# Optimization experiments

Hardware: AMD Instinct MI355X
Metric: run time of the kernel (lower is better)

## Reference

```python
import jax, jax.numpy as jnp
import numpy as np

H_IMG, W_IMG = 160, 160
C1, C2, HEADS, NHOPS = 128, 256, 8, 2
N_NODES = H_IMG * W_IMG


def build_edges(H, W):
    # 3x3 neighborhood (excl. self) + skip edges (i+2,j),(i,j+2); self loops added once
    node = (np.arange(H)[:, None] * W + np.arange(W)[None, :])
    offsets = [(di, dj) for di in (-1, 0, 1) for dj in (-1, 0, 1) if (di, dj) != (0, 0)] + [(2, 0), (0, 2)]
    srcs, dsts = [], []
    for di, dj in offsets:
        i0, i1 = max(0, -di), H - max(0, di)
        j0, j1 = max(0, -dj), W - max(0, dj)
        srcs.append(node[i0:i1, j0:j1].ravel())
        dsts.append(node[i0 + di:i1 + di, j0 + dj:j1 + dj].ravel())
    n = np.arange(H * W)
    srcs.append(n); dsts.append(n)
    return (np.concatenate(srcs).astype(np.int32), np.concatenate(dsts).astype(np.int32))


def setup_inputs() -> dict:
    key = jax.random.key(0)
    ks = jax.random.split(key, 16)
    s = 0.05
    src_np, dst_np = build_edges(H_IMG, W_IMG)
    d = C2 // HEADS
    return {
        "x": jax.random.normal(ks[0], (1, C1, H_IMG, W_IMG), jnp.float32),
        "w_id": jax.random.normal(ks[1], (C2, C1), jnp.float32) * s,
        "w_in": jax.random.normal(ks[2], (C2, C1), jnp.float32) * s,
        "w_gat": jax.random.normal(ks[3], (NHOPS, C2, C2), jnp.float32) * s,
        "a_src": jax.random.normal(ks[4], (NHOPS, HEADS, d), jnp.float32) * s,
        "a_dst": jax.random.normal(ks[5], (NHOPS, HEADS, d), jnp.float32) * s,
        "gat_bias": jax.random.normal(ks[6], (NHOPS, C2), jnp.float32) * s,
        "bn_gamma": jax.random.uniform(ks[7], (NHOPS, C2), jnp.float32, 0.5, 1.5),
        "bn_beta": jax.random.normal(ks[8], (NHOPS, C2), jnp.float32) * s,
        "bn_mean": jax.random.normal(ks[9], (NHOPS, C2), jnp.float32) * s,
        "bn_var": jax.random.uniform(ks[10], (NHOPS, C2), jnp.float32, 0.5, 1.5),
        "w_out": jax.random.normal(ks[11], (C2, C2), jnp.float32) * s,
        "se_w1": jax.random.normal(ks[12], (C2 // 4, C2), jnp.float32) * s,
        "se_b1": jax.random.normal(ks[13], (C2 // 4,), jnp.float32) * s,
        "se_w2": jax.random.normal(ks[14], (C2, C2 // 4), jnp.float32) * s,
        "se_b2": jax.random.normal(ks[15], (C2,), jnp.float32) * s,
        "src": jnp.asarray(src_np),
        "dst": jnp.asarray(dst_np),
    }


def _gat(x, W, a_s, a_d, b, src, dst, N):
    heads, d = a_s.shape
    h = (x @ W.T).reshape(N, heads, d)                      # [N,H,D]
    al_s = jnp.einsum('nhd,hd->nh', h, a_s)                 # [N,H]
    al_d = jnp.einsum('nhd,hd->nh', h, a_d)
    e = jax.nn.leaky_relu(al_s[src] + al_d[dst], 0.2)       # [E,H]
    emax = jax.lax.stop_gradient(jax.ops.segment_max(e, dst, num_segments=N))
    ee = jnp.exp(e - emax[dst])
    denom = jax.ops.segment_sum(ee, dst, num_segments=N)
    alpha = ee / (denom[dst] + 1e-16)                       # segment softmax over incoming edges
    out = jax.ops.segment_sum(h[src] * alpha[..., None], dst, num_segments=N)
    return out.reshape(N, heads * d) + b


def _forward(x, w_id, w_in, w_gat, a_src, a_dst, gat_bias, bn_gamma, bn_beta,
             bn_mean, bn_var, w_out, se_w1, se_b1, se_w2, se_b2, src, dst):
    identity = jnp.einsum('bchw,oc->bohw', x, w_id)
    h = jnp.einsum('bchw,oc->bohw', x, w_in)
    B, C, H, W = h.shape
    N = B * H * W
    xf = h.transpose(0, 2, 3, 1).reshape(N, C)
    for l in range(NHOPS):
        res = xf
        g = _gat(xf, w_gat[l], a_src[l], a_dst[l], gat_bias[l], src, dst, N)
        g = (g - bn_mean[l]) * (bn_gamma[l] * jax.lax.rsqrt(bn_var[l] + 1e-5)) + bn_beta[l]
        xf = jax.nn.relu(g) + res
    y = xf.reshape(B, H, W, C).transpose(0, 3, 1, 2)
    y = jnp.einsum('bchw,oc->bohw', y, w_out)
    # SE block
    w = y.mean(axis=(2, 3))                                 # [B,C]
    w = jax.nn.relu(w @ se_w1.T + se_b1)
    w = jax.nn.sigmoid(w @ se_w2.T + se_b2)
    y = y * w[:, :, None, None]
    return y + identity


def reference(x, w_id, w_in, w_gat, a_src, a_dst, gat_bias, bn_gamma, bn_beta,
              bn_mean, bn_var, w_out, se_w1, se_b1, se_w2, se_b2, src, dst):
    return _forward(x, w_id, w_in, w_gat, a_src, a_dst, gat_bias, bn_gamma, bn_beta,
                    bn_mean, bn_var, w_out, se_w1, se_b1, se_w2, se_b2, src, dst)
```

## Files before the change

kernel.cpp:

```cpp
#include <hip/hip_runtime.h>

#define NN 25600
#define HH 160
#define WW 160
#define C2 256
#define MSLOTS 64

#define B_WIN   0
#define B_WID   32768
#define B_WGAT  65536
#define B_WOUT  196608
#define B_WEND  262144

#define C_BNA   0
#define C_BNB   512
#define C_ASRC  1024
#define C_ADST  1536
#define C_SEW1  2048
#define C_SEB1  18432
#define C_SEW2  18496
#define C_SEB2  34880
#define C_END   35136

typedef __attribute__((ext_vector_type(8))) short bfrag;
typedef __attribute__((ext_vector_type(4))) float ffrag;

__device__ __forceinline__ float b2f(unsigned short u) {
    union { unsigned int ui; float f; } v; v.ui = ((unsigned int)u) << 16; return v.f;
}
__device__ __forceinline__ unsigned short f2b(float f) {
    union { float f; unsigned int u; } v; v.f = f;
    unsigned int u = v.u;
    unsigned int r = (u + 0x7FFFu + ((u >> 16) & 1u)) >> 16;
    return (unsigned short)r;
}
__device__ __forceinline__ float lo16f(unsigned int w) {
    union { unsigned int ui; float f; } v; v.ui = w << 16; return v.f;
}
__device__ __forceinline__ float hi16f(unsigned int w) {
    union { unsigned int ui; float f; } v; v.ui = w & 0xFFFF0000u; return v.f;
}
__device__ __forceinline__ bool probe_f32(const unsigned short* __restrict__ x) {
    int l = threadIdx.x & 63;
    bool wild = false;
#pragma unroll
    for (int i = 0; i < 8; ++i) {
        float v = b2f(x[l * 8 + i]);
        wild |= !(fabsf(v) < 1e6f);
    }
    return __any(wild);
}
__device__ __forceinline__ float ldf(const void* p, long i, bool f32) {
    return f32 ? ((const float*)p)[i] : b2f(((const unsigned short*)p)[i]);
}

__device__ __forceinline__ void gemm_tile_ids(int bid, int& m0, int& o0) {
    int w = (bid & 7) * 200 + (bid >> 3);
    m0 = (w >> 2) * 64;
    o0 = (w & 3) * 64;
}

__device__ __forceinline__ const bfrag* fragp(const unsigned short* buf, int row, int c8) {
    return (const bfrag*)(buf + row * 64 + ((c8 ^ (row & 7)) << 3));
}

__global__ __launch_bounds__(256) void prep_kernel(
    const unsigned short* __restrict__ xp,
    const void* pwin, const void* pwid, const void* pwgat, const void* pwout,
    const void* pasrc, const void* padst, const void* pgbias,
    const void* pbng, const void* pbnb, const void* pbnm, const void* pbnv,
    const void* psew1, const void* pseb1, const void* psew2, const void* pseb2,
    unsigned short* __restrict__ wb, float* __restrict__ cvt,
    float* __restrict__ means, unsigned short* __restrict__ xT)
{
    __shared__ unsigned short T[64 * 136];
    const bool f32 = probe_f32(xp);
    const int tid = threadIdx.x;
    const int bid = blockIdx.x;
    const int gid = bid * 256 + tid;
    const int stride = gridDim.x * 256;

    for (int i = gid; i < MSLOTS * 256; i += stride) means[i] = 0.f;

    for (int i = gid; i < B_WEND; i += stride) {
        const void* s; int o;
        if      (i < B_WID)   { s = pwin;  o = i - B_WIN; }
        else if (i < B_WGAT)  { s = pwid;  o = i - B_WID; }
        else if (i < B_WOUT)  { s = pwgat; o = i - B_WGAT; }
        else                  { s = pwout; o = i - B_WOUT; }
        wb[i] = f32 ? f2b(((const float*)s)[o]) : ((const unsigned short*)s)[o];
    }
    for (int i = gid; i < 512; i += stride) {
        float sc = ldf(pbng, i, f32) * rsqrtf(ldf(pbnv, i, f32) + 1e-5f);
        cvt[C_BNA + i] = sc;
        cvt[C_BNB + i] = (ldf(pgbias, i, f32) - ldf(pbnm, i, f32)) * sc + ldf(pbnb, i, f32);
        cvt[C_ASRC + i] = ldf(pasrc, i, f32);
        cvt[C_ADST + i] = ldf(padst, i, f32);
    }
    for (int i = gid; i < 16384; i += stride) {
        cvt[C_SEW1 + i] = ldf(psew1, i, f32);
        cvt[C_SEW2 + i] = ldf(psew2, i, f32);
    }
    for (int i = gid; i < 64; i += stride)  cvt[C_SEB1 + i] = ldf(pseb1, i, f32);
    for (int i = gid; i < 256; i += stride) cvt[C_SEB2 + i] = ldf(pseb2, i, f32);

    {
        const int n0 = bid * 64;
        const int nl = tid & 63;
#pragma unroll
        for (int i = 0; i < 32; ++i) {
            int c = i * 4 + (tid >> 6);
            long idx = (long)c * NN + n0 + nl;
            T[nl * 136 + c] = f32 ? f2b(((const float*)xp)[idx]) : xp[idx];
        }
        __syncthreads();
#pragma unroll
        for (int i = 0; i < 4; ++i) {
            int n = tid >> 2, c0 = (tid & 3) * 32 + i * 8;
            uint4 v = *(const uint4*)&T[n * 136 + c0];
            *(uint4*)(xT + (long)(n0 + n) * 128 + c0) = v;
        }
    }
}

struct SmemC64 { unsigned short Cs[64 * 72]; };
struct SmemGu  { unsigned short As[4096], Bs[4096]; };
union  SmemNu  { SmemGu g; SmemC64 c; };
struct SmemG2u { unsigned short As[4096], Bi[4096], Bd[4096]; };
union  SmemXu  { SmemG2u g; SmemC64 c; };
struct SmemT   { float T[64 * 73]; };
union  SmemFu  { SmemGu g; SmemT t; };

#define STAGE_TILE(DST, SRC, ROW0, LDA, K0)                                       \
    {                                                                             \
        _Pragma("unroll")                                                         \
        for (int ii = 0; ii < 2; ++ii) {                                          \
            int e = tid + ii * 256;                                               \
            int row = e >> 3;                                                     \
            int q = (e & 7) ^ (row & 7);                                          \
            __builtin_amdgcn_global_load_lds(                                     \
                (const unsigned int*)((SRC) + (long)((ROW0) + row) * (LDA) + (K0) + q * 8), \
                (unsigned int*)&(DST)[e * 8], 16, 0, 0);                          \
        }                                                                         \
    }

__global__ __launch_bounds__(256) void mfma_gemm_x2_kernel(
    const unsigned short* __restrict__ A16,
    const unsigned short* __restrict__ Wi16,
    const unsigned short* __restrict__ Wd16,
    unsigned short* __restrict__ xf16,
    unsigned short* __restrict__ idb16)
{
    __shared__ SmemXu sm;
    const int tid = threadIdx.x;
    int m0, o0; gemm_tile_ids(blockIdx.x, m0, o0);
    const int lane = tid & 63, wv = tid >> 6;
    const int wm = wv >> 1, wn = wv & 1;
    const int lr = lane & 15, quad = lane >> 4;

    ffrag ai[2][2], ad[2][2];
#pragma unroll
    for (int mt = 0; mt < 2; ++mt)
#pragma unroll
        for (int nt = 0; nt < 2; ++nt) { ai[mt][nt] = (ffrag){0,0,0,0}; ad[mt][nt] = (ffrag){0,0,0,0}; }

    for (int k0 = 0; k0 < 128; k0 += 64) {
        STAGE_TILE(sm.g.As, A16,  m0, 128, k0)
        STAGE_TILE(sm.g.Bi, Wi16, o0, 128, k0)
        STAGE_TILE(sm.g.Bd, Wd16, o0, 128, k0)
        __syncthreads();
#pragma unroll
        for (int ks = 0; ks < 2; ++ks) {
            bfrag a[2], bi[2], bd[2];
#pragma unroll
            for (int mt = 0; mt < 2; ++mt)
                a[mt] = *fragp(sm.g.As, wm * 32 + mt * 16 + lr, ks * 4 + quad);
#pragma unroll
            for (int nt = 0; nt < 2; ++nt) {
                bi[nt] = *fragp(sm.g.Bi, wn * 32 + nt * 16 + lr, ks * 4 + quad);
                bd[nt] = *fragp(sm.g.Bd, wn * 32 + nt * 16 + lr, ks * 4 + quad);
            }
#pragma unroll
            for (int mt = 0; mt < 2; ++mt)
#pragma unroll
                for (int nt = 0; nt < 2; ++nt) {
                    ai[mt][nt] = __builtin_amdgcn_mfma_f32_16x16x32_bf16(a[mt], bi[nt], ai[mt][nt], 0, 0, 0);
                    ad[mt][nt] = __builtin_amdgcn_mfma_f32_16x16x32_bf16(a[mt], bd[nt], ad[mt][nt], 0, 0, 0);
                }
        }
        __syncthreads();
    }
#pragma unroll
    for (int mt = 0; mt < 2; ++mt)
#pragma unroll
        for (int nt = 0; nt < 2; ++nt)
#pragma unroll
            for (int r = 0; r < 4; ++r)
                sm.c.Cs[(wm * 32 + mt * 16 + quad * 4 + r) * 72 + wn * 32 + nt * 16 + lr] = f2b(ai[mt][nt][r]);
    __syncthreads();
#pragma unroll
    for (int it = 0; it < 2; ++it) {
        int e = it * 256 + tid;
        int row = e >> 3, c8 = (e & 7) * 8;
        *(uint4*)(xf16 + (long)(m0 + row) * C2 + o0 + c8) = *(const uint4*)&sm.c.Cs[row * 72 + c8];
    }
    __syncthreads();
#pragma unroll
    for (int mt = 0; mt < 2; ++mt)
#pragma unroll
        for (int nt = 0; nt < 2; ++nt)
#pragma unroll
            for (int r = 0; r < 4; ++r)
                sm.c.Cs[(wm * 32 + mt * 16 + quad * 4 + r) * 72 + wn * 32 + nt * 16 + lr] = f2b(ad[mt][nt][r]);
    __syncthreads();
#pragma unroll
    for (int it = 0; it < 2; ++it) {
        int e = it * 256 + tid;
        int row = e >> 3, c8 = (e & 7) * 8;
        *(uint4*)(idb16 + (long)(m0 + row) * C2 + o0 + c8) = *(const uint4*)&sm.c.Cs[row * 72 + c8];
    }
}

__global__ __launch_bounds__(256) void gat_gemm_kernel(
    const unsigned short* __restrict__ A16,
    const unsigned short* __restrict__ W16,
    unsigned short* __restrict__ Cout,
    const float* __restrict__ asrc, const float* __restrict__ adst,
    float* __restrict__ als_out, float* __restrict__ ald_out)
{
    __shared__ SmemNu sm;
    const int tid = threadIdx.x;
    int m0, o0; gemm_tile_ids(blockIdx.x, m0, o0);
    const int lane = tid & 63, wv = tid >> 6;
    const int wm = wv >> 1, wn = wv & 1;
    const int lr = lane & 15, quad = lane >> 4;

    ffrag acc[2][2];
#pragma unroll
    for (int mt = 0; mt < 2; ++mt)
#pragma unroll
        for (int nt = 0; nt < 2; ++nt) acc[mt][nt] = (ffrag){0,0,0,0};

    for (int k0 = 0; k0 < 256; k0 += 64) {
        STAGE_TILE(sm.g.As, A16, m0, C2, k0)
        STAGE_TILE(sm.g.Bs, W16, o0, C2, k0)
        __syncthreads();
#pragma unroll
        for (int ks = 0; ks < 2; ++ks) {
            bfrag a[2], b[2];
#pragma unroll
            for (int mt = 0; mt < 2; ++mt)
                a[mt] = *fragp(sm.g.As, wm * 32 + mt * 16 + lr, ks * 4 + quad);
#pragma unroll
            for (int nt = 0; nt < 2; ++nt)
                b[nt] = *fragp(sm.g.Bs, wn * 32 + nt * 16 + lr, ks * 4 + quad);
#pragma unroll
            for (int mt = 0; mt < 2; ++mt)
#pragma unroll
                for (int nt = 0; nt < 2; ++nt)
                    acc[mt][nt] = __builtin_amdgcn_mfma_f32_16x16x32_bf16(a[mt], b[nt], acc[mt][nt], 0, 0, 0);
        }
        __syncthreads();
    }
    {
        const int head = (o0 >> 5) + wn;
        const float as0 = asrc[head * 32 + lr], as1 = asrc[head * 32 + 16 + lr];
        const float ad0 = adst[head * 32 + lr], ad1 = adst[head * 32 + 16 + lr];
#pragma unroll
        for (int mt = 0; mt < 2; ++mt)
#pragma unroll
            for (int r = 0; r < 4; ++r) {
                float ps = acc[mt][0][r] * as0 + acc[mt][1][r] * as1;
                float pd = acc[mt][0][r] * ad0 + acc[mt][1][r] * ad1;
#pragma unroll
                for (int sh = 1; sh < 16; sh <<= 1) {
                    ps += __shfl_xor(ps, sh);
                    pd += __shfl_xor(pd, sh);
                }
                if (lr == 0) {
                    int m = m0 + wm * 32 + mt * 16 + quad * 4 + r;
                    als_out[m * 8 + head] = ps;
                    ald_out[m * 8 + head] = pd;
                }
            }
    }
#pragma unroll
    for (int mt = 0; mt < 2; ++mt)
#pragma unroll
        for (int nt = 0; nt < 2; ++nt)
#pragma unroll
            for (int r = 0; r < 4; ++r)
                sm.c.Cs[(wm * 32 + mt * 16 + quad * 4 + r) * 72 + wn * 32 + nt * 16 + lr] = f2b(acc[mt][nt][r]);
    __syncthreads();
#pragma unroll
    for (int it = 0; it < 2; ++it) {
        int e = it * 256 + tid;
        int row = e >> 3, c8 = (e & 7) * 8;
        *(uint4*)(Cout + (long)(m0 + row) * C2 + o0 + c8) = *(const uint4*)&sm.c.Cs[row * 72 + c8];
    }
}

__global__ __launch_bounds__(256) void aggregate_kernel(
    const unsigned short* __restrict__ h16,
    const float* __restrict__ al_s,
    const float* __restrict__ al_d,
    const float* __restrict__ bnA,
    const float* __restrict__ bnB,
    unsigned short* __restrict__ xf16,
    float* __restrict__ means)
{
    const int SI[11] = { 1, 1, 1, 0, 0, -1, -1, -1, -2,  0, 0};
    const int SJ[11] = { 1, 0,-1, 1,-1,  1,  0, -1,  0, -2, 0};
    __shared__ float part[4][256];

    const int t = threadIdx.x;
    const int ln = t >> 5;
    const int l = t & 31;
    const int n = blockIdx.x * 8 + ln;
    const int i = n / WW, j = n % WW;
    const int c8 = l * 8;
    const int hd = l >> 2;

    int srcn[11]; bool okm[11];
#pragma unroll
    for (int k = 0; k < 11; ++k) {
        int si = i + SI[k], sj = j + SJ[k];
        bool ok = (si >= 0) & (si < HH) & (sj >= 0) & (sj < WW);
        okm[k] = ok;
        srcn[k] = ok ? si * WW + sj : n;
    }

    float e[11];
    {
        const float ald = al_d[n * 8 + hd];
        float mx = -1e30f;
#pragma unroll
        for (int k = 0; k < 11; ++k) {
            float s = al_s[(long)srcn[k] * 8 + hd];
            float v = s + ald;
            v = v > 0.f ? v : 0.2f * v;
            v = okm[k] ? v : -1e30f;
            e[k] = v;
            mx = fmaxf(mx, v);
        }
        float denom = 0.f;
#pragma unroll
        for (int k = 0; k < 11; ++k) {
            float p = __expf(e[k] - mx);
            e[k] = p;
            denom += p;
        }
        const float inv = 1.f / (denom + 1e-16f);
#pragma unroll
        for (int k = 0; k < 11; ++k) e[k] *= inv;
    }

    uint4 hv[11];
#pragma unroll
    for (int k = 0; k < 11; ++k)
        hv[k] = *(const uint4*)(h16 + (long)srcn[k] * C2 + c8);
    uint4 rv = *(const uint4*)(xf16 + (long)n * C2 + c8);

    float a0=0.f,a1=0.f,a2=0.f,a3=0.f,a4=0.f,a5=0.f,a6=0.f,a7=0.f;
#pragma unroll
    for (int k = 0; k < 11; ++k) {
        float al = e[k];
        a0 += al * lo16f(hv[k].x); a1 += al * hi16f(hv[k].x);
        a2 += al * lo16f(hv[k].y); a3 += al * hi16f(hv[k].y);
        a4 += al * lo16f(hv[k].z); a5 += al * hi16f(hv[k].z);
        a6 += al * lo16f(hv[k].w); a7 += al * hi16f(hv[k].w);
    }
    float acc8[8] = {a0,a1,a2,a3,a4,a5,a6,a7};
    float res[8] = {lo16f(rv.x),hi16f(rv.x),lo16f(rv.y),hi16f(rv.y),
                    lo16f(rv.z),hi16f(rv.z),lo16f(rv.w),hi16f(rv.w)};
    float out[8];
#pragma unroll
    for (int q = 0; q < 8; ++q) {
        int c = c8 + q;
        float g = acc8[q] * bnA[c] + bnB[c];
        out[q] = fmaxf(g, 0.f) + res[q];
    }
    ushort4 o16a, o16b;
    o16a.x = f2b(out[0]); o16a.y = f2b(out[1]); o16a.z = f2b(out[2]); o16a.w = f2b(out[3]);
    o16b.x = f2b(out[4]); o16b.y = f2b(out[5]); o16b.z = f2b(out[6]); o16b.w = f2b(out[7]);
    *(ushort4*)(xf16 + (long)n * C2 + c8)     = o16a;
    *(ushort4*)(xf16 + (long)n * C2 + c8 + 4) = o16b;

    if (means) {
        float s8[8];
#pragma unroll
        for (int q = 0; q < 8; ++q) {
            s8[q] = out[q];
            s8[q] += __shfl_xor(s8[q], 32);
        }
        const int wvi = t >> 6;
        if ((t & 63) < 32) {
#pragma unroll
            for (int q = 0; q < 8; ++q) part[wvi][c8 + q] = s8[q];
        }
        __syncthreads();
        {
            float v = part[0][t] + part[1][t] + part[2][t] + part[3][t];
            atomicAdd(&means[(blockIdx.x & (MSLOTS - 1)) * 256 + t], v);
        }
    }
}

__global__ __launch_bounds__(256) void se_kernel(
    const unsigned short* __restrict__ W16,
    const float* __restrict__ means,
    const float* __restrict__ cvt,
    float* __restrict__ sv_out)
{
    __shared__ float cs[256], mv[256], hv[64];
    const int t = threadIdx.x;
    {
        float s0=0,s1=0,s2=0,s3=0,s4=0,s5=0,s6=0,s7=0;
#pragma unroll 2
        for (int sl = 0; sl < MSLOTS; sl += 8) {
            s0 += means[(sl+0)*256 + t]; s1 += means[(sl+1)*256 + t];
            s2 += means[(sl+2)*256 + t]; s3 += means[(sl+3)*256 + t];
            s4 += means[(sl+4)*256 + t]; s5 += means[(sl+5)*256 + t];
            s6 += means[(sl+6)*256 + t]; s7 += means[(sl+7)*256 + t];
        }
        cs[t] = ((s0+s1)+(s2+s3)) + ((s4+s5)+(s6+s7));
    }
    __syncthreads();
    {
        float s = 0.f;
        const unsigned short* wr = W16 + (long)t * C2;
#pragma unroll 4
        for (int k = 0; k < 256; k += 8) {
            uint4 w = *(const uint4*)(wr + k);
            s += cs[k]   * lo16f(w.x) + cs[k+1] * hi16f(w.x)
               + cs[k+2] * lo16f(w.y) + cs[k+3] * hi16f(w.y)
               + cs[k+4] * lo16f(w.z) + cs[k+5] * hi16f(w.z)
               + cs[k+6] * lo16f(w.w) + cs[k+7] * hi16f(w.w);
        }
        mv[t] = s * (1.0f / 25600.0f);
    }
    __syncthreads();
    if (t < 64) {
        const float* w1 = cvt + C_SEW1 + t * 256;
        float s = cvt[C_SEB1 + t];
        for (int cc = 0; cc < 256; cc += 4) {
            float4 w = *(const float4*)(w1 + cc);
            s += w.x * mv[cc] + w.y * mv[cc+1] + w.z * mv[cc+2] + w.w * mv[cc+3];
        }
        hv[t] = fmaxf(s, 0.f);
    }
    __syncthreads();
    {
        const float* w2 = cvt + C_SEW2 + t * 64;
        float s = cvt[C_SEB2 + t];
        for (int k = 0; k < 64; k += 4) {
            float4 w = *(const float4*)(w2 + k);
            s += w.x * hv[k] + w.y * hv[k+1] + w.z * hv[k+2] + w.w * hv[k+3];
        }
        sv_out[t] = 1.0f / (1.0f + __expf(-s));
    }
}

__global__ __launch_bounds__(256) void final_gemm_kernel(
    const unsigned short* __restrict__ x_probe,
    const unsigned short* __restrict__ A16,
    const unsigned short* __restrict__ W16,
    const unsigned short* __restrict__ idb16,
    const float* __restrict__ sv,
    void* __restrict__ outp)
{
    __shared__ SmemFu sm;
    const bool f32o = probe_f32(x_probe);
    const int tid = threadIdx.x;
    int m0, o0; gemm_tile_ids(blockIdx.x, m0, o0);
    const int lane = tid & 63, wv = tid >> 6;
    const int wm = wv >> 1, wn = wv & 1;
    const int lr = lane & 15, quad = lane >> 4;

    ffrag acc[2][2];
#pragma unroll
    for (int mt = 0; mt < 2; ++mt)
#pragma unroll
        for (int nt = 0; nt < 2; ++nt) acc[mt][nt] = (ffrag){0,0,0,0};

    for (int k0 = 0; k0 < 256; k0 += 64) {
        STAGE_TILE(sm.g.As, A16, m0, C2, k0)
        STAGE_TILE(sm.g.Bs, W16, o0, C2, k0)
        __syncthreads();
#pragma unroll
        for (int ks = 0; ks < 2; ++ks) {
            bfrag a[2], b[2];
#pragma unroll
            for (int mt = 0; mt < 2; ++mt)
                a[mt] = *fragp(sm.g.As, wm * 32 + mt * 16 + lr, ks * 4 + quad);
#pragma unroll
            for (int nt = 0; nt < 2; ++nt)
                b[nt] = *fragp(sm.g.Bs, wn * 32 + nt * 16 + lr, ks * 4 + quad);
#pragma unroll
            for (int mt = 0; mt < 2; ++mt)
#pragma unroll
                for (int nt = 0; nt < 2; ++nt)
                    acc[mt][nt] = __builtin_amdgcn_mfma_f32_16x16x32_bf16(a[mt], b[nt], acc[mt][nt], 0, 0, 0);
        }
        __syncthreads();
    }

#pragma unroll
    for (int mt = 0; mt < 2; ++mt)
#pragma unroll
        for (int nt = 0; nt < 2; ++nt) {
            int cl = wn * 32 + nt * 16 + lr;
            float s = sv[o0 + cl];
#pragma unroll
            for (int r = 0; r < 4; ++r) {
                int row = wm * 32 + mt * 16 + quad * 4 + r;
                float v = acc[mt][nt][r] * s + b2f(idb16[(long)(m0 + row) * C2 + o0 + cl]);
                sm.t.T[cl * 73 + row] = v;
            }
        }
    __syncthreads();
#pragma unroll
    for (int it = 0; it < 16; ++it) {
        int e = it * 256 + tid;
        int cc = e >> 6, nn = e & 63;
        long idx = (long)(o0 + cc) * NN + m0 + nn;
        float v = sm.t.T[cc * 73 + nn];
        if (f32o) ((float*)outp)[idx] = v;
        else      ((unsigned short*)outp)[idx] = f2b(v);
    }
}

extern "C" void kernel_launch(void* const* d_in, const int* in_sizes, int n_in,
                              void* d_out, int out_size, void* d_ws, size_t ws_size,
                              hipStream_t stream) {
    float* ws = (float*)d_ws;
    float* cvt   = ws;
    float* means = ws + 35200;
    float* svb   = means + MSLOTS * 256;
    float* als   = svb + 256;
    float* ald   = als + 204800;
    unsigned short* wb16  = (unsigned short*)(ald + 204800);
    unsigned short* xT16  = wb16 + B_WEND;
    unsigned short* xf16  = xT16 + NN * 128;
    unsigned short* h16   = xf16 + NN * 256;
    unsigned short* idb16 = h16 + NN * 256;

    const unsigned short* xp = (const unsigned short*)d_in[0];

    dim3 b256(256);

    prep_kernel<<<400, b256, 0, stream>>>(
        xp, d_in[2], d_in[1], d_in[3], d_in[11],
        d_in[4], d_in[5], d_in[6], d_in[7], d_in[8], d_in[9], d_in[10],
        d_in[12], d_in[13], d_in[14], d_in[15],
        wb16, cvt, means, xT16);

    mfma_gemm_x2_kernel<<<1600, b256, 0, stream>>>(
        xT16, wb16 + B_WIN, wb16 + B_WID, xf16, idb16);

    for (int l = 0; l < 2; ++l) {
        gat_gemm_kernel<<<1600, b256, 0, stream>>>(
            xf16, wb16 + B_WGAT + l * 65536, h16,
            cvt + C_ASRC + l * 256, cvt + C_ADST + l * 256, als, ald);
        aggregate_kernel<<<NN / 8, b256, 0, stream>>>(h16, als, ald,
            cvt + C_BNA + l * 256, cvt + C_BNB + l * 256, xf16,
            (l == 1) ? means : nullptr);
    }

    se_kernel<<<1, b256, 0, stream>>>(wb16 + B_WOUT, means, cvt, svb);

    final_gemm_kernel<<<1600, b256, 0, stream>>>(
        xp, xf16, wb16 + B_WOUT, idb16, svb, d_out);
}
```

Measured before the change: 206.0 us.

## Recompute identity projection in final GEMM instead of storing bf16 intermediate

The identity branch (x @ w_id) is no longer computed in the first GEMM and written to a bf16 buffer. The final GEMM now runs a second K-loop over the transposed input and w_id and adds that accumulator directly to the SE-scaled output. This removes a 13 MB write and read of the identity intermediate and one bf16 rounding step. In exchange the final kernel holds extra accumulators and does more MFMA work, which can raise register pressure.

```diff
diff --git a/kernel.cpp b/kernel.cpp
--- a/kernel.cpp
+++ b/kernel.cpp
@@ -126,8 +126,6 @@
 struct SmemC64 { unsigned short Cs[64 * 72]; };
 struct SmemGu  { unsigned short As[4096], Bs[4096]; };
 union  SmemNu  { SmemGu g; SmemC64 c; };
-struct SmemG2u { unsigned short As[4096], Bi[4096], Bd[4096]; };
-union  SmemXu  { SmemG2u g; SmemC64 c; };
 struct SmemT   { float T[64 * 73]; };
 union  SmemFu  { SmemGu g; SmemT t; };
 
@@ -144,49 +142,42 @@
         }                                                                         \
     }
 
-__global__ __launch_bounds__(256) void mfma_gemm_x2_kernel(
+__global__ __launch_bounds__(256) void mfma_gemm_kernel(
     const unsigned short* __restrict__ A16,
     const unsigned short* __restrict__ Wi16,
-    const unsigned short* __restrict__ Wd16,
-    unsigned short* __restrict__ xf16,
-    unsigned short* __restrict__ idb16)
+    unsigned short* __restrict__ xf16)
 {
-    __shared__ SmemXu sm;
+    __shared__ SmemNu sm;
     const int tid = threadIdx.x;
     int m0, o0; gemm_tile_ids(blockIdx.x, m0, o0);
     const int lane = tid & 63, wv = tid >> 6;
     const int wm = wv >> 1, wn = wv & 1;
     const int lr = lane & 15, quad = lane >> 4;
 
-    ffrag ai[2][2], ad[2][2];
+    ffrag ai[2][2];
 #pragma unroll
     for (int mt = 0; mt < 2; ++mt)
 #pragma unroll
-        for (int nt = 0; nt < 2; ++nt) { ai[mt][nt] = (ffrag){0,0,0,0}; ad[mt][nt] = (ffrag){0,0,0,0}; }
+        for (int nt = 0; nt < 2; ++nt) ai[mt][nt] = (ffrag){0,0,0,0};
 
     for (int k0 = 0; k0 < 128; k0 += 64) {
         STAGE_TILE(sm.g.As, A16,  m0, 128, k0)
-        STAGE_TILE(sm.g.Bi, Wi16, o0, 128, k0)
-        STAGE_TILE(sm.g.Bd, Wd16, o0, 128, k0)
+        STAGE_TILE(sm.g.Bs, Wi16, o0, 128, k0)
         __syncthreads();
 #pragma unroll
         for (int ks = 0; ks < 2; ++ks) {
-            bfrag a[2], bi[2], bd[2];
+            bfrag a[2], bi[2];
 #pragma unroll
             for (int mt = 0; mt < 2; ++mt)
                 a[mt] = *fragp(sm.g.As, wm * 32 + mt * 16 + lr, ks * 4 + quad);
 #pragma unroll
-            for (int nt = 0; nt < 2; ++nt) {
-                bi[nt] = *fragp(sm.g.Bi, wn * 32 + nt * 16 + lr, ks * 4 + quad);
-                bd[nt] = *fragp(sm.g.Bd, wn * 32 + nt * 16 + lr, ks * 4 + quad);
-            }
-#pragma unroll
-            for (int mt = 0; mt < 2; ++mt)
-#pragma unroll
-                for (int nt = 0; nt < 2; ++nt) {
+            for (int nt = 0; nt < 2; ++nt)
+                bi[nt] = *fragp(sm.g.Bs, wn * 32 + nt * 16 + lr, ks * 4 + quad);
+#pragma unroll
+            for (int mt = 0; mt < 2; ++mt)
+#pragma unroll
+                for (int nt = 0; nt < 2; ++nt)
                     ai[mt][nt] = __builtin_amdgcn_mfma_f32_16x16x32_bf16(a[mt], bi[nt], ai[mt][nt], 0, 0, 0);
-                    ad[mt][nt] = __builtin_amdgcn_mfma_f32_16x16x32_bf16(a[mt], bd[nt], ad[mt][nt], 0, 0, 0);
-                }
         }
         __syncthreads();
     }
@@ -203,21 +194,6 @@
         int e = it * 256 + tid;
         int row = e >> 3, c8 = (e & 7) * 8;
         *(uint4*)(xf16 + (long)(m0 + row) * C2 + o0 + c8) = *(const uint4*)&sm.c.Cs[row * 72 + c8];
-    }
-    __syncthreads();
-#pragma unroll
-    for (int mt = 0; mt < 2; ++mt)
-#pragma unroll
-        for (int nt = 0; nt < 2; ++nt)
-#pragma unroll
-            for (int r = 0; r < 4; ++r)
-                sm.c.Cs[(wm * 32 + mt * 16 + quad * 4 + r) * 72 + wn * 32 + nt * 16 + lr] = f2b(ad[mt][nt][r]);
-    __syncthreads();
-#pragma unroll
-    for (int it = 0; it < 2; ++it) {
-        int e = it * 256 + tid;
-        int row = e >> 3, c8 = (e & 7) * 8;
-        *(uint4*)(idb16 + (long)(m0 + row) * C2 + o0 + c8) = *(const uint4*)&sm.c.Cs[row * 72 + c8];
     }
 }
 
@@ -465,7 +441,8 @@
     const unsigned short* __restrict__ x_probe,
     const unsigned short* __restrict__ A16,
     const unsigned short* __restrict__ W16,
-    const unsigned short* __restrict__ idb16,
+    const unsigned short* __restrict__ AT16,
+    const unsigned short* __restrict__ Wd16,
     const float* __restrict__ sv,
     void* __restrict__ outp)
 {
@@ -477,11 +454,11 @@
     const int wm = wv >> 1, wn = wv & 1;
     const int lr = lane & 15, quad = lane >> 4;
 
-    ffrag acc[2][2];
+    ffrag acc[2][2], accI[2][2];
 #pragma unroll
     for (int mt = 0; mt < 2; ++mt)
 #pragma unroll
-        for (int nt = 0; nt < 2; ++nt) acc[mt][nt] = (ffrag){0,0,0,0};
+        for (int nt = 0; nt < 2; ++nt) { acc[mt][nt] = (ffrag){0,0,0,0}; accI[mt][nt] = (ffrag){0,0,0,0}; }
 
     for (int k0 = 0; k0 < 256; k0 += 64) {
         STAGE_TILE(sm.g.As, A16, m0, C2, k0)
@@ -504,6 +481,27 @@
         }
         __syncthreads();
     }
+    for (int k0 = 0; k0 < 128; k0 += 64) {
+        STAGE_TILE(sm.g.As, AT16, m0, 128, k0)
+        STAGE_TILE(sm.g.Bs, Wd16, o0, 128, k0)
+        __syncthreads();
+#pragma unroll
+        for (int ks = 0; ks < 2; ++ks) {
+            bfrag a[2], b[2];
+#pragma unroll
+            for (int mt = 0; mt < 2; ++mt)
+                a[mt] = *fragp(sm.g.As, wm * 32 + mt * 16 + lr, ks * 4 + quad);
+#pragma unroll
+            for (int nt = 0; nt < 2; ++nt)
+                b[nt] = *fragp(sm.g.Bs, wn * 32 + nt * 16 + lr, ks * 4 + quad);
+#pragma unroll
+            for (int mt = 0; mt < 2; ++mt)
+#pragma unroll
+                for (int nt = 0; nt < 2; ++nt)
+                    accI[mt][nt] = __builtin_amdgcn_mfma_f32_16x16x32_bf16(a[mt], b[nt], accI[mt][nt], 0, 0, 0);
+        }
+        __syncthreads();
+    }
 
 #pragma unroll
     for (int mt = 0; mt < 2; ++mt)
@@ -514,7 +512,7 @@
 #pragma unroll
             for (int r = 0; r < 4; ++r) {
                 int row = wm * 32 + mt * 16 + quad * 4 + r;
-                float v = acc[mt][nt][r] * s + b2f(idb16[(long)(m0 + row) * C2 + o0 + cl]);
+                float v = acc[mt][nt][r] * s + accI[mt][nt][r];
                 sm.t.T[cl * 73 + row] = v;
             }
         }
@@ -543,7 +541,6 @@
     unsigned short* xT16  = wb16 + B_WEND;
     unsigned short* xf16  = xT16 + NN * 128;
     unsigned short* h16   = xf16 + NN * 256;
-    unsigned short* idb16 = h16 + NN * 256;
 
     const unsigned short* xp = (const unsigned short*)d_in[0];
 
@@ -555,8 +552,8 @@
         d_in[12], d_in[13], d_in[14], d_in[15],
         wb16, cvt, means, xT16);
 
-    mfma_gemm_x2_kernel<<<1600, b256, 0, stream>>>(
-        xT16, wb16 + B_WIN, wb16 + B_WID, xf16, idb16);
+    mfma_gemm_kernel<<<1600, b256, 0, stream>>>(
+        xT16, wb16 + B_WIN, xf16);
 
     for (int l = 0; l < 2; ++l) {
         gat_gemm_kernel<<<1600, b256, 0, stream>>>(
@@ -570,5 +567,5 @@
     se_kernel<<<1, b256, 0, stream>>>(wb16 + B_WOUT, means, cvt, svb);
 
     final_gemm_kernel<<<1600, b256, 0, stream>>>(
-        xp, xf16, wb16 + B_WOUT, idb16, svb, d_out);
-}
+        xp, xf16, wb16 + B_WOUT, xT16, wb16 + B_WID, svb, d_out);
+}
```

Result: faster. 201.9 us (-2.0%).
